# Kernel tuning notes

Hardware: AMD Instinct MI355X
Metric: run time of the kernel (lower is better)

## Reference

```python
import jax, jax.numpy as jnp
import numpy as np

N = 100000      # num nodes
R = 32          # num relations
E = 3200000     # num edges
F_IN = 128      # feat_len
H = 16          # hidden dim (hard-coded in source)
C = 8           # num classes


def setup_inputs() -> dict:
    key = jax.random.key(0)
    k1, k2, k3, k4, k5 = jax.random.split(key, 5)
    emb = jax.random.normal(k1, (N, F_IN), dtype=jnp.float32)
    W1 = jax.random.normal(k2, (R, F_IN, H), dtype=jnp.float32) * 0.05
    W2 = jax.random.normal(k3, (R, H, C), dtype=jnp.float32) * 0.05
    edge_index = jax.random.randint(k4, (2, E), 0, N, dtype=jnp.int64)
    edge_type = jax.random.randint(k5, (E,), 0, R, dtype=jnp.int64)
    return {"emb": emb, "W1": W1, "W2": W2,
            "edge_index": edge_index, "edge_type": edge_type}


def _rgcn_layer(x, W, src, dst, etype, edge_norm):
    # x: [N, Fin], W: [R, Fin, Fout]
    # Transform once per relation, then gather per edge (avoids [E,Fin,Fout]).
    xw = jnp.einsum('nf,rfo->rno', x, W)          # [R, N, Fout]
    msg = xw[etype, src] * edge_norm[:, None]      # [E, Fout]
    return jax.ops.segment_sum(msg, dst, num_segments=N)  # [N, Fout]


def reference(emb, W1, W2, edge_index, edge_type):
    src, dst = edge_index[0], edge_index[1]
    # PyG RGCNConv aggr='mean': normalize by per-(dst, relation) in-degree.
    key_idx = dst * R + edge_type                              # [E]
    deg = jax.ops.segment_sum(jnp.ones((E,), emb.dtype), key_idx,
                              num_segments=N * R)              # [N*R]
    edge_norm = 1.0 / jnp.maximum(deg, 1.0)
    edge_norm = edge_norm[key_idx]                             # [E]

    h = jax.nn.relu(_rgcn_layer(emb, W1, src, dst, edge_type, edge_norm))
    h = _rgcn_layer(h, W2, src, dst, edge_type, edge_norm)
    return jax.nn.log_softmax(h, axis=1)
```

## Files before the change

### kernel.cpp

```cpp
#include <hip/hip_runtime.h>
#include <hip/hip_bf16.h>
#include <math.h>

#define N_NODES 100000
#define R 32
#define E_EDGES 3200000
#define F_IN 128
#define HDIM 16
#define CDIM 8
#define NOUT 512
#define M_PAD 100032
#define NBUCK 391
#define CAP 9216
#define KEYS 8192
#define P1CHUNK 8192
#define CVT_BLKS 6252
#define PREP_BLKS 128
#define FRONT_GRID (NBUCK + CVT_BLKS + PREP_BLKS)
#define GEMM_BLKS 1563
#define MID_GRID (NBUCK + GEMM_BLKS)

typedef __attribute__((ext_vector_type(8))) short bf16x8;
typedef __attribute__((ext_vector_type(4))) float f32x4;
typedef __attribute__((ext_vector_type(2))) _Float16 f16x2;

static __device__ __forceinline__ unsigned short f2bf(float f) {
    unsigned int u = __float_as_uint(f);
    unsigned int r = (u + 0x7FFFu + ((u >> 16) & 1u)) >> 16;
    return (unsigned short)r;
}
static __device__ __forceinline__ float bfl(unsigned x) {
    return __uint_as_float(x << 16);
}
static __device__ __forceinline__ float bfh(unsigned x) {
    return __uint_as_float(x & 0xFFFF0000u);
}

#if __has_builtin(__builtin_amdgcn_fdot2)
static __device__ __forceinline__ float FDOT2(f16x2 a, f16x2 b, float c) {
    return __builtin_amdgcn_fdot2(a, b, c, false);
}
#else
static __device__ __forceinline__ float FDOT2(f16x2 a, f16x2 b, float c) {
    return c + (float)a.x * (float)b.x + (float)a.y * (float)b.y;
}
#endif

__global__ __launch_bounds__(512) void k_front(const int* __restrict__ src,
                                               const int* __restrict__ dst,
                                               const int* __restrict__ et,
                                               const float* __restrict__ emb,
                                               const float* __restrict__ W1,
                                               int* __restrict__ gcursor,
                                               unsigned int* __restrict__ ebuf,
                                               unsigned short* __restrict__ ebf,
                                               unsigned short* __restrict__ BmT) {
    __shared__ int sh[3 * NBUCK];
    int b = blockIdx.x, t = threadIdx.x;
    if (b < NBUCK) {
        int* hist = sh;
        int* rank = sh + NBUCK;
        int* base = sh + 2 * NBUCK;
        for (int j = t; j < NBUCK; j += 512) { hist[j] = 0; rank[j] = 0; }
        __syncthreads();
        int e0 = b * P1CHUNK;
        int e1 = e0 + P1CHUNK; if (e1 > E_EDGES) e1 = E_EDGES;
        int n4 = (e1 - e0) >> 2;
        const int4* d4 = (const int4*)(dst + e0);
        const int4* s4 = (const int4*)(src + e0);
        const int4* t4 = (const int4*)(et + e0);
        for (int i = t; i < n4; i += 512) {
            int4 v = d4[i];
            atomicAdd(&hist[v.x >> 8], 1);
            atomicAdd(&hist[v.y >> 8], 1);
            atomicAdd(&hist[v.z >> 8], 1);
            atomicAdd(&hist[v.w >> 8], 1);
        }
        __syncthreads();
        for (int j = t; j < NBUCK; j += 512)
            base[j] = hist[j] ? atomicAdd(&gcursor[j], hist[j]) : 0;
        __syncthreads();
        for (int i = t; i < n4; i += 512) {
            int4 dv = d4[i];
            int4 sv = s4[i];
            int4 tv = t4[i];
            int ds[4] = {dv.x, dv.y, dv.z, dv.w};
            int ss[4] = {sv.x, sv.y, sv.z, sv.w};
            int ts[4] = {tv.x, tv.y, tv.z, tv.w};
            #pragma unroll
            for (int u = 0; u < 4; ++u) {
                int d = ds[u];
                int bk = d >> 8;
                unsigned pk = ((unsigned)(d & 255) << 22) | ((unsigned)ts[u] << 17)
                            | (unsigned)ss[u];
                int lr = atomicAdd(&rank[bk], 1);
                ebuf[(size_t)bk * CAP + base[bk] + lr] = pk;
            }
        }
    } else if (b < NBUCK + CVT_BLKS) {
        size_t base = ((size_t)(b - NBUCK) * 512 + t) * 4;
        int row = (int)(base >> 7);
        ushort4 o;
        if (row < N_NODES) {
            float4 a = *(const float4*)(emb + base);
            o.x = f2bf(a.x); o.y = f2bf(a.y); o.z = f2bf(a.z); o.w = f2bf(a.w);
        } else {
            o.x = o.y = o.z = o.w = 0;
        }
        *(ushort4*)(ebf + base) = o;
    } else {
        int i = (b - NBUCK - CVT_BLKS) * 512 + t;
        int n = i >> 7;
        int f = i & 127;
        int r = n >> 4;
        int o = n & 15;
        BmT[i] = f2bf(W1[r * (F_IN * HDIM) + f * HDIM + o]);
    }
}

__global__ __launch_bounds__(256) void k_mid(const unsigned int* __restrict__ ebuf,
                                             const int* __restrict__ gcursor,
                                             int2* __restrict__ rse,
                                             unsigned int* __restrict__ elist,
                                             const unsigned short* __restrict__ Abf,
                                             const unsigned short* __restrict__ BmT,
                                             unsigned short* __restrict__ C) {
    __shared__ __align__(16) char smem[34816 + 64];
    int b = blockIdx.x, t = threadIdx.x;
    if (b < NBUCK) {
        unsigned int* cnt = (unsigned int*)smem;
        int* wsum = (int*)(smem + 32768);
        int cntE = gcursor[b];
        size_t e0 = (size_t)b * CAP;
        #pragma unroll
        for (int j = 0; j < KEYS / 256; ++j) cnt[t + j * 256] = 0;
        __syncthreads();
        for (int i = t; i < cntE; i += 256)
            atomicAdd(&cnt[ebuf[e0 + i] >> 17], 1u);
        __syncthreads();
        int kbase = t * (KEYS / 256);
        int s = 0;
        #pragma unroll
        for (int j = 0; j < KEYS / 256; ++j) s += (int)cnt[kbase + j];
        int lane = t & 63, wv = t >> 6;
        int sc = s;
        #pragma unroll
        for (int off = 1; off < 64; off <<= 1) {
            int v = __shfl_up(sc, off, 64);
            if (lane >= off) sc += v;
        }
        if (lane == 63) wsum[wv] = sc;
        __syncthreads();
        if (t == 0) {
            int a = 0;
            #pragma unroll
            for (int w = 0; w < 4; ++w) { int v = wsum[w]; wsum[w] = a; a += v; }
        }
        __syncthreads();
        int run = wsum[wv] + sc - s;
        #pragma unroll
        for (int j = 0; j < KEYS / 256; ++j) {
            unsigned v = cnt[kbase + j];
            unsigned lc = v > 1023u ? 1023u : v;
            cnt[kbase + j] = (unsigned)run | (lc << 20);
            run += (int)v;
        }
        __syncthreads();
        {
            int d = b * 256 + t;
            if (d < N_NODES) {
                int rs = (int)(cnt[t * 32] & 0xFFFFFu);
                int re = (t < 255) ? (int)(cnt[(t + 1) * 32] & 0xFFFFFu) : cntE;
                rse[d] = make_int2((int)e0 + rs, (int)e0 + re);
            }
        }
        __syncthreads();
        for (int i = t; i < cntE; i += 256) {
            unsigned pk = ebuf[e0 + i];
            int key = pk >> 17;
            unsigned vv = atomicAdd(&cnt[key], 1u);
            int pos = (int)(vv & 0xFFFFFu);
            unsigned len = (vv >> 20) & 1023u;
            elist[e0 + pos] = (pk & 0x3FFFFFu) | (len << 22);
        }
    } else {
        unsigned short* As = (unsigned short*)smem;
        unsigned short* Bs = (unsigned short*)(smem + 17408);
        int row0 = (b - NBUCK) * 64;
        #pragma unroll
        for (int j = 0; j < 4; ++j) {
            int idx = t + j * 256;
            int r = idx >> 4;
            int u = idx & 15;
            float4 v = *(const float4*)(Abf + (size_t)(row0 + r) * F_IN + u * 8);
            *(float4*)(&As[r * 136 + u * 8]) = v;
        }
        int w = t >> 6;
        int lane = t & 63;
        int q = lane >> 4;
        int mr = lane & 15;
        const unsigned short* ap = &As[(w * 16 + mr) * 136 + q * 8];
        for (int col0 = 0; col0 < NOUT; col0 += 64) {
            __syncthreads();
            #pragma unroll
            for (int j = 0; j < 4; ++j) {
                int idx = t + j * 256;
                int r = idx >> 4;
                int u = idx & 15;
                float4 v = *(const float4*)(BmT + (size_t)(col0 + r) * F_IN + u * 8);
                *(float4*)(&Bs[r * 136 + u * 8]) = v;
            }
            __syncthreads();
            f32x4 acc[4] = {};
            #pragma unroll
            for (int kk = 0; kk < 4; ++kk) {
                bf16x8 af = *(const bf16x8*)(ap + kk * 32);
                #pragma unroll
                for (int tt = 0; tt < 4; ++tt) {
                    bf16x8 bf = *(const bf16x8*)(&Bs[(tt * 16 + mr) * 136 + q * 8 + kk * 32]);
                    acc[tt] = __builtin_amdgcn_mfma_f32_16x16x32_bf16(af, bf, acc[tt], 0, 0, 0);
                }
            }
            #pragma unroll
            for (int tt = 0; tt < 4; ++tt) {
                #pragma unroll
                for (int j = 0; j < 4; ++j) {
                    int row = row0 + w * 16 + q * 4 + j;
                    C[(size_t)row * NOUT + col0 + tt * 16 + mr] = f2bf(acc[tt][j]);
                }
            }
        }
    }
}

__global__ __launch_bounds__(256) void k_gather1(const int2* __restrict__ rse,
                                                 const unsigned int* __restrict__ elist,
                                                 const unsigned short* __restrict__ xw1,
                                                 _Float16* __restrict__ h) {
    __shared__ float nlut[1024];
    int t = threadIdx.x;
    for (int j = t; j < 1024; j += 256) nlut[j] = 1.0f / (float)(j ? j : 1);
    __syncthreads();
    int g = t >> 3;
    int c = t & 7;
    int d = blockIdx.x * 32 + g;
    if (d >= N_NODES) return;
    int2 rr = rse[d];
    int i = rr.x, end = rr.y;
    float a0 = 0.f, a1 = 0.f, b0 = 0.f, b1 = 0.f;
    float c0 = 0.f, c1 = 0.f, e0 = 0.f, e1 = 0.f;
    for (; i + 3 < end; i += 4) {
        unsigned pk0 = elist[i];
        unsigned pk1 = elist[i + 1];
        unsigned pk2 = elist[i + 2];
        unsigned pk3 = elist[i + 3];
        unsigned x0 = *(const unsigned*)(xw1 + (size_t)(pk0 & 0x1FFFF) * NOUT + ((pk0 >> 17) & 31) * HDIM + c * 2);
        unsigned x1 = *(const unsigned*)(xw1 + (size_t)(pk1 & 0x1FFFF) * NOUT + ((pk1 >> 17) & 31) * HDIM + c * 2);
        unsigned x2 = *(const unsigned*)(xw1 + (size_t)(pk2 & 0x1FFFF) * NOUT + ((pk2 >> 17) & 31) * HDIM + c * 2);
        unsigned x3 = *(const unsigned*)(xw1 + (size_t)(pk3 & 0x1FFFF) * NOUT + ((pk3 >> 17) & 31) * HDIM + c * 2);
        float n0 = nlut[pk0 >> 22], n1 = nlut[pk1 >> 22];
        float n2 = nlut[pk2 >> 22], n3 = nlut[pk3 >> 22];
        a0 += bfl(x0) * n0; a1 += bfh(x0) * n0;
        b0 += bfl(x1) * n1; b1 += bfh(x1) * n1;
        c0 += bfl(x2) * n2; c1 += bfh(x2) * n2;
        e0 += bfl(x3) * n3; e1 += bfh(x3) * n3;
    }
    for (; i < end; ++i) {
        unsigned pk = elist[i];
        unsigned x = *(const unsigned*)(xw1 + (size_t)(pk & 0x1FFFF) * NOUT + ((pk >> 17) & 31) * HDIM + c * 2);
        float nm = nlut[pk >> 22];
        a0 += bfl(x) * nm; a1 += bfh(x) * nm;
    }
    f16x2 o;
    o.x = (_Float16)fmaxf(a0 + b0 + c0 + e0, 0.f);
    o.y = (_Float16)fmaxf(a1 + b1 + c1 + e1, 0.f);
    *(f16x2*)(h + (size_t)d * HDIM + c * 2) = o;
}

__global__ __launch_bounds__(256) void k_gather2(const int2* __restrict__ rse,
                                                 const unsigned int* __restrict__ elist,
                                                 const _Float16* __restrict__ h,
                                                 const float* __restrict__ W2,
                                                 float* __restrict__ out) {
    __shared__ f16x2 w2cl[8 * 264];
    __shared__ f16x2 nlutH[1024];
    int t = threadIdx.x;
    for (int j = t; j < 1024; j += 256) {
        float nm = 1.0f / (float)(j ? j : 1);
        f16x2 p; p.x = (_Float16)nm; p.y = (_Float16)nm;
        nlutH[j] = p;
    }
    #pragma unroll
    for (int j = 0; j < 8; ++j) {
        int idx = t + j * 256;
        int ch = idx >> 8;
        int r = (idx >> 3) & 31;
        int cls = idx & 7;
        f16x2 p;
        p.x = (_Float16)W2[r * 128 + (2 * ch) * 8 + cls];
        p.y = (_Float16)W2[r * 128 + (2 * ch + 1) * 8 + cls];
        w2cl[ch * 264 + r * 8 + cls] = p;
    }
    __syncthreads();

    int g = t >> 3;
    int ch = t & 7;
    int d = blockIdx.x * 32 + g;
    if (d >= N_NODES) return;
    const f16x2* wbase = &w2cl[ch * 264];
    int2 rr = rse[d];
    int i = rr.x, end = rr.y;
    float acc[8] = {};
    for (; i + 3 < end; i += 4) {
        unsigned pk0 = elist[i];
        unsigned pk1 = elist[i + 1];
        unsigned pk2 = elist[i + 2];
        unsigned pk3 = elist[i + 3];
        f16x2 h0 = *(const f16x2*)(h + (size_t)(pk0 & 0x1FFFF) * HDIM + ch * 2);
        f16x2 h1 = *(const f16x2*)(h + (size_t)(pk1 & 0x1FFFF) * HDIM + ch * 2);
        f16x2 h2 = *(const f16x2*)(h + (size_t)(pk2 & 0x1FFFF) * HDIM + ch * 2);
        f16x2 h3 = *(const f16x2*)(h + (size_t)(pk3 & 0x1FFFF) * HDIM + ch * 2);
        h0 *= nlutH[pk0 >> 22];
        h1 *= nlutH[pk1 >> 22];
        h2 *= nlutH[pk2 >> 22];
        h3 *= nlutH[pk3 >> 22];
        const f16x2* w0 = wbase + ((pk0 >> 17) & 31) * 8;
        const f16x2* w1 = wbase + ((pk1 >> 17) & 31) * 8;
        const f16x2* w2 = wbase + ((pk2 >> 17) & 31) * 8;
        const f16x2* w3 = wbase + ((pk3 >> 17) & 31) * 8;
        #pragma unroll
        for (int k = 0; k < 8; ++k) {
            acc[k] = FDOT2(h0, w0[k], acc[k]);
            acc[k] = FDOT2(h1, w1[k], acc[k]);
            acc[k] = FDOT2(h2, w2[k], acc[k]);
            acc[k] = FDOT2(h3, w3[k], acc[k]);
        }
    }
    for (; i < end; ++i) {
        unsigned pk = elist[i];
        f16x2 hv = *(const f16x2*)(h + (size_t)(pk & 0x1FFFF) * HDIM + ch * 2);
        hv *= nlutH[pk >> 22];
        const f16x2* wp = wbase + ((pk >> 17) & 31) * 8;
        #pragma unroll
        for (int k = 0; k < 8; ++k)
            acc[k] = FDOT2(hv, wp[k], acc[k]);
    }
    #pragma unroll
    for (int mask = 1; mask < 8; mask <<= 1) {
        #pragma unroll
        for (int k = 0; k < 8; ++k)
            acc[k] += __shfl_xor(acc[k], mask, 8);
    }
    float v = acc[ch];
    float m = v;
    #pragma unroll
    for (int mask = 1; mask < 8; mask <<= 1)
        m = fmaxf(m, __shfl_xor(m, mask, 8));
    float ex = expf(v - m);
    float ssumv = ex;
    #pragma unroll
    for (int mask = 1; mask < 8; mask <<= 1)
        ssumv += __shfl_xor(ssumv, mask, 8);
    out[(size_t)d * CDIM + ch] = v - m - logf(ssumv);
}

extern "C" void kernel_launch(void* const* d_in, const int* in_sizes, int n_in,
                              void* d_out, int out_size, void* d_ws, size_t ws_size,
                              hipStream_t stream) {
    const float* emb = (const float*)d_in[0];
    const float* W1  = (const float*)d_in[1];
    const float* W2  = (const float*)d_in[2];
    const int* ei    = (const int*)d_in[3];
    const int* et    = (const int*)d_in[4];
    const int* srcp  = ei;
    const int* dstp  = ei + E_EDGES;

    char* ws = (char*)d_ws;
    size_t off = 0;
    #define ALIGN256(x) (((x) + 255) & ~(size_t)255)
    int* gcursor     = (int*)(ws + off); off = ALIGN256(off + 512 * 4);
    int2* rse        = (int2*)(ws + off); off = ALIGN256(off + ((size_t)N_NODES + 8) * 8);
    unsigned int* ebuf  = (unsigned int*)(ws + off); off = ALIGN256(off + (size_t)NBUCK * CAP * 4);
    unsigned int* elist = (unsigned int*)(ws + off); off = ALIGN256(off + (size_t)NBUCK * CAP * 4);
    unsigned short* BmT  = (unsigned short*)(ws + off); off = ALIGN256(off + (size_t)NOUT * F_IN * 2);
    unsigned short* ebf  = (unsigned short*)(ws + off); off = ALIGN256(off + (size_t)M_PAD * F_IN * 2);
    unsigned short* xw1  = (unsigned short*)(ws + off); off = ALIGN256(off + (size_t)M_PAD * NOUT * 2);
    _Float16* h          = (_Float16*)(ws + off);       off = ALIGN256(off + (size_t)N_NODES * HDIM * 2);
    float* out = (float*)d_out;

    hipMemsetAsync(gcursor, 0, 512 * 4, stream);

    k_front<<<FRONT_GRID, 512, 0, stream>>>(srcp, dstp, et, emb, W1, gcursor, ebuf, ebf, BmT);
    k_mid<<<MID_GRID, 256, 0, stream>>>(ebuf, gcursor, rse, elist, ebf, BmT, xw1);
    k_gather1<<<(N_NODES + 31) / 32, 256, 0, stream>>>(rse, elist, xw1, h);
    k_gather2<<<(N_NODES + 31) / 32, 256, 0, stream>>>(rse, elist, h, W2, out);
}
```

Measured before the change: 307.1 us.

## Cache packed edges in registers and double k_mid block size and GEMM tile

In the front bucketing pass, each thread packs its edges into a register array during the histogram pass, so the scatter pass re-reads only dst instead of dst, src and type. k_mid now runs 512-thread blocks: the counting-sort buckets use twice the threads, and the GEMM blocks cover 128 rows instead of 64, halving the grid and the number of times the B tile is reloaded. This raises LDS use to about 52 KB per block and the per-thread register count, which can reduce occupancy. M_PAD and the conversion grid grow to match the 128-row tiles.

New measurement: 297.0 us. 1.03x faster.

```diff
diff --git a/kernel.cpp b/kernel.cpp
--- a/kernel.cpp
+++ b/kernel.cpp
@@ -9,15 +9,15 @@
 #define HDIM 16
 #define CDIM 8
 #define NOUT 512
-#define M_PAD 100032
+#define M_PAD 100096
 #define NBUCK 391
 #define CAP 9216
 #define KEYS 8192
 #define P1CHUNK 8192
-#define CVT_BLKS 6252
+#define CVT_BLKS 6256
 #define PREP_BLKS 128
 #define FRONT_GRID (NBUCK + CVT_BLKS + PREP_BLKS)
-#define GEMM_BLKS 1563
+#define GEMM_BLKS 782
 #define MID_GRID (NBUCK + GEMM_BLKS)
 
 typedef __attribute__((ext_vector_type(8))) short bf16x8;
@@ -69,18 +69,9 @@
         const int4* d4 = (const int4*)(dst + e0);
         const int4* s4 = (const int4*)(src + e0);
         const int4* t4 = (const int4*)(et + e0);
-        for (int i = t; i < n4; i += 512) {
-            int4 v = d4[i];
-            atomicAdd(&hist[v.x >> 8], 1);
-            atomicAdd(&hist[v.y >> 8], 1);
-            atomicAdd(&hist[v.z >> 8], 1);
-            atomicAdd(&hist[v.w >> 8], 1);
-        }
-        __syncthreads();
-        for (int j = t; j < NBUCK; j += 512)
-            base[j] = hist[j] ? atomicAdd(&gcursor[j], hist[j]) : 0;
-        __syncthreads();
-        for (int i = t; i < n4; i += 512) {
+        unsigned pkreg[16];
+        int j = 0;
+        for (int i = t; i < n4; i += 512, ++j) {
             int4 dv = d4[i];
             int4 sv = s4[i];
             int4 tv = t4[i];
@@ -89,12 +80,24 @@
             int ts[4] = {tv.x, tv.y, tv.z, tv.w};
             #pragma unroll
             for (int u = 0; u < 4; ++u) {
-                int d = ds[u];
-                int bk = d >> 8;
-                unsigned pk = ((unsigned)(d & 255) << 22) | ((unsigned)ts[u] << 17)
-                            | (unsigned)ss[u];
+                atomicAdd(&hist[ds[u] >> 8], 1);
+                pkreg[j * 4 + u] = ((unsigned)(ds[u] & 255) << 22)
+                                 | ((unsigned)ts[u] << 17) | (unsigned)ss[u];
+            }
+        }
+        __syncthreads();
+        for (int k = t; k < NBUCK; k += 512)
+            base[k] = hist[k] ? atomicAdd(&gcursor[k], hist[k]) : 0;
+        __syncthreads();
+        j = 0;
+        for (int i = t; i < n4; i += 512, ++j) {
+            int4 dv = d4[i];
+            int ds[4] = {dv.x, dv.y, dv.z, dv.w};
+            #pragma unroll
+            for (int u = 0; u < 4; ++u) {
+                int bk = ds[u] >> 8;
                 int lr = atomicAdd(&rank[bk], 1);
-                ebuf[(size_t)bk * CAP + base[bk] + lr] = pk;
+                ebuf[(size_t)bk * CAP + base[bk] + lr] = pkreg[j * 4 + u];
             }
         }
     } else if (b < NBUCK + CVT_BLKS) {
@@ -118,14 +121,14 @@
     }
 }
 
-__global__ __launch_bounds__(256) void k_mid(const unsigned int* __restrict__ ebuf,
+__global__ __launch_bounds__(512) void k_mid(const unsigned int* __restrict__ ebuf,
                                              const int* __restrict__ gcursor,
                                              int2* __restrict__ rse,
                                              unsigned int* __restrict__ elist,
                                              const unsigned short* __restrict__ Abf,
                                              const unsigned short* __restrict__ BmT,
                                              unsigned short* __restrict__ C) {
-    __shared__ __align__(16) char smem[34816 + 64];
+    __shared__ __align__(16) char smem[52224 + 64];
     int b = blockIdx.x, t = threadIdx.x;
     if (b < NBUCK) {
         unsigned int* cnt = (unsigned int*)smem;
@@ -133,15 +136,15 @@
         int cntE = gcursor[b];
         size_t e0 = (size_t)b * CAP;
         #pragma unroll
-        for (int j = 0; j < KEYS / 256; ++j) cnt[t + j * 256] = 0;
-        __syncthreads();
-        for (int i = t; i < cntE; i += 256)
+        for (int j = 0; j < KEYS / 512; ++j) cnt[t + j * 512] = 0;
+        __syncthreads();
+        for (int i = t; i < cntE; i += 512)
             atomicAdd(&cnt[ebuf[e0 + i] >> 17], 1u);
         __syncthreads();
-        int kbase = t * (KEYS / 256);
+        int kbase = t * (KEYS / 512);
         int s = 0;
         #pragma unroll
-        for (int j = 0; j < KEYS / 256; ++j) s += (int)cnt[kbase + j];
+        for (int j = 0; j < KEYS / 512; ++j) s += (int)cnt[kbase + j];
         int lane = t & 63, wv = t >> 6;
         int sc = s;
         #pragma unroll
@@ -154,19 +157,19 @@
         if (t == 0) {
             int a = 0;
             #pragma unroll
-            for (int w = 0; w < 4; ++w) { int v = wsum[w]; wsum[w] = a; a += v; }
+            for (int w = 0; w < 8; ++w) { int v = wsum[w]; wsum[w] = a; a += v; }
         }
         __syncthreads();
         int run = wsum[wv] + sc - s;
         #pragma unroll
-        for (int j = 0; j < KEYS / 256; ++j) {
+        for (int j = 0; j < KEYS / 512; ++j) {
             unsigned v = cnt[kbase + j];
             unsigned lc = v > 1023u ? 1023u : v;
             cnt[kbase + j] = (unsigned)run | (lc << 20);
             run += (int)v;
         }
         __syncthreads();
-        {
+        if (t < 256) {
             int d = b * 256 + t;
             if (d < N_NODES) {
                 int rs = (int)(cnt[t * 32] & 0xFFFFFu);
@@ -175,7 +178,7 @@
             }
         }
         __syncthreads();
-        for (int i = t; i < cntE; i += 256) {
+        for (int i = t; i < cntE; i += 512) {
             unsigned pk = ebuf[e0 + i];
             int key = pk >> 17;
             unsigned vv = atomicAdd(&cnt[key], 1u);
@@ -185,11 +188,11 @@
         }
     } else {
         unsigned short* As = (unsigned short*)smem;
-        unsigned short* Bs = (unsigned short*)(smem + 17408);
-        int row0 = (b - NBUCK) * 64;
+        unsigned short* Bs = (unsigned short*)(smem + 34816);
+        int row0 = (b - NBUCK) * 128;
         #pragma unroll
         for (int j = 0; j < 4; ++j) {
-            int idx = t + j * 256;
+            int idx = t + j * 512;
             int r = idx >> 4;
             int u = idx & 15;
             float4 v = *(const float4*)(Abf + (size_t)(row0 + r) * F_IN + u * 8);
@@ -203,8 +206,8 @@
         for (int col0 = 0; col0 < NOUT; col0 += 64) {
             __syncthreads();
             #pragma unroll
-            for (int j = 0; j < 4; ++j) {
-                int idx = t + j * 256;
+            for (int j = 0; j < 2; ++j) {
+                int idx = t + j * 512;
                 int r = idx >> 4;
                 int u = idx & 15;
                 float4 v = *(const float4*)(BmT + (size_t)(col0 + r) * F_IN + u * 8);
@@ -391,7 +394,7 @@
     hipMemsetAsync(gcursor, 0, 512 * 4, stream);
 
     k_front<<<FRONT_GRID, 512, 0, stream>>>(srcp, dstp, et, emb, W1, gcursor, ebuf, ebf, BmT);
-    k_mid<<<MID_GRID, 256, 0, stream>>>(ebuf, gcursor, rse, elist, ebf, BmT, xw1);
+    k_mid<<<MID_GRID, 512, 0, stream>>>(ebuf, gcursor, rse, elist, ebf, BmT, xw1);
     k_gather1<<<(N_NODES + 31) / 32, 256, 0, stream>>>(rse, elist, xw1, h);
     k_gather2<<<(N_NODES + 31) / 32, 256, 0, stream>>>(rse, elist, h, W2, out);
 }
```
